# Kernel optimization log

Measured on AMD Instinct MI355X. Metric: run time of the kernel, lower is better.

## Reference

```python
import jax, jax.numpy as jnp
import numpy as np

D = 128          # hidden_channels
NU = 50000       # num user nodes
NI = 50000       # num item nodes
E = 600000       # edges per edge type
SLOPE = 0.01     # F.leaky_relu default negative_slope


def setup_inputs() -> dict:
    key = jax.random.key(0)
    ks = jax.random.split(key, 24)
    ws = 1.0 / np.sqrt(D)  # xavier-ish scale

    def W2(i):  # stacked [n_layers=2, D, D] weight
        return jax.random.normal(ks[i], (2, D, D), jnp.float32) * ws

    def B2(i):  # stacked [2, D] bias
        return jax.random.normal(ks[i], (2, D), jnp.float32) * 0.01

    inp = {
        "x_user": jax.random.normal(ks[0], (NU, D), jnp.float32),
        "x_item": jax.random.normal(ks[1], (NI, D), jnp.float32),
        # row 0 = src indices, row 1 = dst indices
        "ei_ui": jax.random.randint(ks[2], (2, E), 0, NU),  # user -> item (dst in [0,NI))
        "ei_iu": jax.random.randint(ks[3], (2, E), 0, NI),  # item -> user (dst in [0,NU))
        # per-node-type q/k/v Linear params, stacked over the 2 layers
        "q_w_user": W2(4),  "q_b_user": B2(5),
        "k_w_user": W2(6),  "k_b_user": B2(7),
        "v_w_user": W2(8),  "v_b_user": B2(9),
        "q_w_item": W2(10), "q_b_item": B2(11),
        "k_w_item": W2(12), "k_b_item": B2(13),
        "v_w_item": W2(14), "v_b_item": B2(15),
        # per-edge-type bilinear W, stacked over the 2 layers
        "W_ui": W2(16),
        "W_iu": W2(17),
    }
    return inp


def _edge_agg(x_src, x_dst, qw, qb, kw, kb, vw, vb, W, src, dst, n_dst):
    # torch Linear: x @ w.T + b
    q = x_src @ qw.T + qb            # [Nsrc, D]
    k = x_dst @ kw.T + kb            # [Ndst, D]
    v = x_src @ vw.T + vb            # [Nsrc, D]
    qW = q @ W                       # project on nodes (cheaper than per-edge)
    # per-edge bilinear score q_src . W . k_dst / sqrt(D)
    score = jnp.sum(qW[src] * k[dst], axis=-1) * (1.0 / np.sqrt(D))  # [E]
    alpha = jax.nn.softmax(jax.nn.leaky_relu(score, SLOPE))          # softmax over edges
    msg = alpha[:, None] * v[src]                                    # [E, D]
    return jax.ops.segment_sum(msg, dst, num_segments=n_dst)


def _layer(x_u, x_i, ei_ui, ei_iu, p, l):
    # edge type (user, rates, item): q/v from src type (user), k from dst type (item)
    agg_i = _edge_agg(x_u, x_i,
                      p["q_w_user"][l], p["q_b_user"][l],
                      p["k_w_item"][l], p["k_b_item"][l],
                      p["v_w_user"][l], p["v_b_user"][l],
                      p["W_ui"][l], ei_ui[0], ei_ui[1], NI)
    # edge type (item, rev_rates, user)
    agg_u = _edge_agg(x_i, x_u,
                      p["q_w_item"][l], p["q_b_item"][l],
                      p["k_w_user"][l], p["k_b_user"][l],
                      p["v_w_item"][l], p["v_b_item"][l],
                      p["W_iu"][l], ei_iu[0], ei_iu[1], NU)
    # out_dict initialized with x_dst.clone(), then scatter_add
    return x_u + agg_u, x_i + agg_i


def reference(x_user, x_item, ei_ui, ei_iu,
              q_w_user, q_b_user, k_w_user, k_b_user, v_w_user, v_b_user,
              q_w_item, q_b_item, k_w_item, k_b_item, v_w_item, v_b_item,
              W_ui, W_iu):
    p = dict(q_w_user=q_w_user, q_b_user=q_b_user, k_w_user=k_w_user,
             k_b_user=k_b_user, v_w_user=v_w_user, v_b_user=v_b_user,
             q_w_item=q_w_item, q_b_item=q_b_item, k_w_item=k_w_item,
             k_b_item=k_b_item, v_w_item=v_w_item, v_b_item=v_b_item,
             W_ui=W_ui, W_iu=W_iu)
    x_u, x_i = _layer(x_user, x_item, ei_ui, ei_iu, p, 0)  # conv1
    x_u, x_i = _layer(x_u, x_i, ei_ui, ei_iu, p, 1)        # conv2
    return jnp.concatenate([x_u, x_i], axis=0)  # [NU+NI, D]
```

## Files before the change

### kernel.cpp

```cpp
#include <hip/hip_runtime.h>
#include <stdint.h>

#define D 128

typedef __attribute__((ext_vector_type(8))) short bf16x8;
typedef __attribute__((ext_vector_type(4))) float f32x4;
typedef __attribute__((ext_vector_type(2))) float f32x2;
typedef unsigned short u16;
typedef unsigned char u8;
typedef unsigned int u32;

static __device__ __forceinline__ float b2f(u16 u) {
  return __uint_as_float(((unsigned)u) << 16);
}
static __device__ __forceinline__ u16 f2b(float f) {
  unsigned u = __float_as_uint(f);
  return (u16)((u + 0x7fffu + ((u >> 16) & 1u)) >> 16);
}

#if defined(__has_builtin)
#if __has_builtin(__builtin_amdgcn_cvt_pk_f32_fp8) && __has_builtin(__builtin_amdgcn_cvt_pk_fp8_f32)
#define HW_FP8 1
#endif
#endif

static __device__ __forceinline__ u8 enc_fp8(float f) {
#ifdef HW_FP8
  int p = __builtin_amdgcn_cvt_pk_fp8_f32(f, 0.f, 0, false);
  return (u8)(p & 0xff);
#else
  float a = fabsf(f);
  unsigned s = (__float_as_uint(f) >> 31) << 7;
  if (a < 7.8125e-3f) {
    int m = (int)(a * 512.f + 0.5f);
    if (m > 7) m = 7;
    return (u8)(s | m);
  }
  int e; float mant = frexpf(a, &e);
  int E = e + 6;
  int m = (int)((2.f * mant - 1.f) * 8.f + 0.5f);
  if (m == 8) { m = 0; E++; }
  if (E > 15 || (E == 15 && m > 6)) { E = 15; m = 6; }
  if (E < 1) return (u8)s;
  return (u8)(s | (E << 3) | m);
#endif
}

static __device__ __forceinline__ float dec1_fp8(u8 b) {
  int e = (b >> 3) & 15, m = b & 7;
  float mag = e ? ldexpf((float)(8 + m), e - 10) : ldexpf((float)m, -9);
  return (b & 128) ? -mag : mag;
}

static __device__ __forceinline__ void dec8_fp8(u32 lo, u32 hi, float* o) {
#ifdef HW_FP8
  f32x2 a = __builtin_amdgcn_cvt_pk_f32_fp8((int)lo, false);
  f32x2 b = __builtin_amdgcn_cvt_pk_f32_fp8((int)lo, true);
  f32x2 c = __builtin_amdgcn_cvt_pk_f32_fp8((int)hi, false);
  f32x2 d = __builtin_amdgcn_cvt_pk_f32_fp8((int)hi, true);
  o[0] = a.x; o[1] = a.y; o[2] = b.x; o[3] = b.y;
  o[4] = c.x; o[5] = c.y; o[6] = d.x; o[7] = d.y;
#else
  u32 w[2] = {lo, hi};
  u8* p = (u8*)w;
#pragma unroll
  for (int i = 0; i < 8; ++i) o[i] = dec1_fp8(p[i]);
#endif
}

__global__ void prep_fused(const float* __restrict__ qwu, const float* __restrict__ qbu,
                           const float* __restrict__ qwi, const float* __restrict__ qbi,
                           const float* __restrict__ Wui, const float* __restrict__ Wiu,
                           u16* __restrict__ Mt, float* __restrict__ bq) {
  int c = blockIdx.y, d = blockIdx.x, j = threadIdx.x;
  int l = c & 1, type = c >> 1;
  const float* qw = (type ? qwi : qwu) + l * D * D;
  const float* qb = (type ? qbi : qbu) + l * D;
  const float* W  = (type ? Wiu : Wui) + l * D * D;
  float acc = 0.f;
  for (int cc = 0; cc < D; ++cc) acc += qw[cc * D + d] * W[cc * D + j];
  Mt[((size_t)c * D + j) * D + d] = f2b(acc);
  if (d == 0) {
    float ba = 0.f;
    for (int cc = 0; cc < D; ++cc) ba += qb[cc] * W[cc * D + j];
    bq[c * D + j] = ba;
  }
}

__global__ void cast_w(const float* __restrict__ kwu, const float* __restrict__ kwi,
                       const float* __restrict__ vwu, const float* __restrict__ vwi,
                       u16* __restrict__ Wb) {
  int y = blockIdx.y;
  const float* s = (y == 0) ? kwu : (y == 1) ? kwi : (y == 2) ? vwu : vwi;
  int i = blockIdx.x * 256 + threadIdx.x;
  Wb[(size_t)y * 2 * D * D + i] = f2b(s[i]);
}

__global__ void cast_x(const float* __restrict__ x, u16* __restrict__ xb, int n2) {
  int i = blockIdx.x * 256 + threadIdx.x;
  if (i < n2) {
    float2 v = ((const float2*)x)[i];
    ((unsigned*)xb)[i] = (unsigned)f2b(v.x) | ((unsigned)f2b(v.y) << 16);
  }
}

__global__ void zero_i(int* __restrict__ p, int n) {
  int i = blockIdx.x * 256 + threadIdx.x;
  if (i < n) p[i] = 0;
}

__global__ __launch_bounds__(256) void bhist(const int* __restrict__ dui,
                                             const int* __restrict__ diu,
                                             int* __restrict__ cnt_ui,
                                             int* __restrict__ cnt_iu, int E) {
  __shared__ int h[256];
  int t = threadIdx.x;
  h[t] = 0;
  __syncthreads();
  const int* dp = blockIdx.y ? diu : dui;
  int e0 = blockIdx.x * 1024;
#pragma unroll
  for (int i = 0; i < 4; ++i) {
    int e = e0 + i * 256 + t;
    if (e < E) atomicAdd(&h[dp[e] >> 8], 1);
  }
  __syncthreads();
  int* out = blockIdx.y ? cnt_iu : cnt_ui;
  if (h[t]) atomicAdd(&out[t], h[t]);
}

__global__ __launch_bounds__(256) void bscan(const int* __restrict__ cnt_ui,
                                             const int* __restrict__ cnt_iu,
                                             int* __restrict__ base_ui, int* __restrict__ base_iu,
                                             int* __restrict__ cur_ui, int* __restrict__ cur_iu,
                                             int* __restrict__ rp_ui, int* __restrict__ rp_iu,
                                             int nb_ui, int nb_iu, int n_ui, int n_iu, int E) {
  __shared__ int sh[256];
  int t = threadIdx.x;
  int v = (t < nb_ui) ? cnt_ui[t] : 0;
  sh[t] = v;
  __syncthreads();
  for (int off = 1; off < 256; off <<= 1) {
    int u = (t >= off) ? sh[t - off] : 0;
    __syncthreads();
    sh[t] += u;
    __syncthreads();
  }
  int ex = sh[t] - v;
  if (t < nb_ui) { base_ui[t] = ex; cur_ui[t] = ex; }
  if (t == 0) { base_ui[nb_ui] = E; rp_ui[n_ui] = E; }
  __syncthreads();
  v = (t < nb_iu) ? cnt_iu[t] : 0;
  sh[t] = v;
  __syncthreads();
  for (int off = 1; off < 256; off <<= 1) {
    int u = (t >= off) ? sh[t - off] : 0;
    __syncthreads();
    sh[t] += u;
    __syncthreads();
  }
  ex = sh[t] - v;
  if (t < nb_iu) { base_iu[t] = ex; cur_iu[t] = ex; }
  if (t == 0) { base_iu[nb_iu] = E; rp_iu[n_iu] = E; }
}

__global__ __launch_bounds__(256) void bscatter(
    const int* __restrict__ sui, const int* __restrict__ dui,
    const int* __restrict__ siu, const int* __restrict__ diu,
    int* __restrict__ cur_ui, int* __restrict__ cur_iu,
    u32* __restrict__ bb_ui, u32* __restrict__ bb_iu, int E) {
  __shared__ int h[256], rbase[256], c2[256];
  int t = threadIdx.x;
  const int* sp = blockIdx.y ? siu : sui;
  const int* dp = blockIdx.y ? diu : dui;
  int* gc = blockIdx.y ? cur_iu : cur_ui;
  u32* bb = blockIdx.y ? bb_iu : bb_ui;
  h[t] = 0;
  c2[t] = 0;
  __syncthreads();
  int e0 = blockIdx.x * 1024;
  u32 pr[4];
  int bk[4];
  bool act[4];
#pragma unroll
  for (int i = 0; i < 4; ++i) {
    int e = e0 + i * 256 + t;
    act[i] = e < E;
    if (act[i]) {
      int s = sp[e], d2 = dp[e];
      pr[i] = ((u32)d2 << 16) | (u32)s;
      bk[i] = d2 >> 8;
      atomicAdd(&h[bk[i]], 1);
    }
  }
  __syncthreads();
  if (h[t]) rbase[t] = atomicAdd(&gc[t], h[t]);
  __syncthreads();
#pragma unroll
  for (int i = 0; i < 4; ++i) {
    if (act[i]) {
      int r = atomicAdd(&c2[bk[i]], 1);
      bb[rbase[bk[i]] + r] = pr[i];
    }
  }
}

__global__ __launch_bounds__(256) void bsort(
    const u32* __restrict__ bb_ui, const u32* __restrict__ bb_iu,
    const int* __restrict__ base_ui, const int* __restrict__ base_iu,
    int* __restrict__ rp_ui, int* __restrict__ rp_iu,
    int* __restrict__ cs_ui, int* __restrict__ cs_iu,
    int nb_ui, int n_ui, int n_iu) {
  int b = blockIdx.x;
  const u32* bb; const int* base; int* rp; int* cs; int n;
  if (b < nb_ui) { bb = bb_ui; base = base_ui; rp = rp_ui; cs = cs_ui; n = n_ui; }
  else { b -= nb_ui; bb = bb_iu; base = base_iu; rp = rp_iu; cs = cs_iu; n = n_iu; }
  int lo = base[b], hi = base[b + 1];
  __shared__ int h[256], sh[256], cur[256];
  int t = threadIdx.x;
  h[t] = 0;
  __syncthreads();
  for (int j = lo + t; j < hi; j += 256) atomicAdd(&h[(bb[j] >> 16) & 255], 1);
  __syncthreads();
  int v = h[t];
  sh[t] = v;
  __syncthreads();
  for (int off = 1; off < 256; off <<= 1) {
    int u = (t >= off) ? sh[t - off] : 0;
    __syncthreads();
    sh[t] += u;
    __syncthreads();
  }
  int ex = lo + sh[t] - v;
  int gd = (b << 8) + t;
  if (gd < n) rp[gd] = ex;
  cur[t] = ex;
  __syncthreads();
  for (int j = lo + t; j < hi; j += 256) {
    u32 pr = bb[j];
    int p = atomicAdd(&cur[(pr >> 16) & 255], 1);
    cs[p] = (int)(pr & 0xffffu);
  }
}

__global__ __launch_bounds__(256) void gemm3(
    const u16* __restrict__ xu, const u16* __restrict__ xi,
    const u16* __restrict__ wqu, const u16* __restrict__ wku, const u16* __restrict__ wvu,
    const float* __restrict__ bqu, const float* __restrict__ bku, const float* __restrict__ bvu,
    const u16* __restrict__ wqi, const u16* __restrict__ wki, const u16* __restrict__ wvi,
    const float* __restrict__ bqi, const float* __restrict__ bki, const float* __restrict__ bvi,
    u8* __restrict__ Tqv_u, u16* __restrict__ Tk_u,
    u8* __restrict__ Tqv_i, u16* __restrict__ Tk_i,
    int gu, int nu, int ni) {
  __shared__ __align__(16) u16 wlds[128 * 136];
  int bx = blockIdx.x, y = blockIdx.y;
  bool item = bx >= gu;
  if (item) bx -= gu;
  const u16* x = item ? xi : xu;
  int nrows = item ? ni : nu;
  const u16* wt; const float* bias;
  if (y == 0)      { wt = item ? wqi : wqu; bias = item ? bqi : bqu; }
  else if (y == 1) { wt = item ? wki : wku; bias = item ? bki : bku; }
  else             { wt = item ? wvi : wvu; bias = item ? bvi : bvu; }
  u8* Tqv = item ? Tqv_i : Tqv_u;
  u16* Tk = item ? Tk_i : Tk_u;

  int t = threadIdx.x;
#pragma unroll
  for (int i = 0; i < 8; ++i) {
    int idx = t + 256 * i;
    int n = idx >> 4, kc = idx & 15;
    ((bf16x8*)wlds)[n * 17 + kc] = ((const bf16x8*)wt)[idx];
  }
  __syncthreads();
  int wave = t >> 6, lane = t & 63;
  int m = lane & 15, quad = lane >> 4;
  int row0 = bx * 64 + wave * 16;
  int arow = row0 + m;
  const bf16x8* xv = (const bf16x8*)(x + (size_t)(arow < nrows ? arow : 0) * D);
  f32x4 acc[8];
#pragma unroll
  for (int n = 0; n < 8; ++n) acc[n] = (f32x4){0.f, 0.f, 0.f, 0.f};
#pragma unroll
  for (int kk = 0; kk < 4; ++kk) {
    bf16x8 a = xv[kk * 4 + quad];
#pragma unroll
    for (int n = 0; n < 8; ++n) {
      bf16x8 b = ((const bf16x8*)wlds)[(n * 16 + m) * 17 + kk * 4 + quad];
      acc[n] = __builtin_amdgcn_mfma_f32_16x16x32_bf16(a, b, acc[n], 0, 0, 0);
    }
  }
  if (y == 1) {
#pragma unroll
    for (int n = 0; n < 8; ++n) {
      float bb = bias[n * 16 + m];
#pragma unroll
      for (int r = 0; r < 4; ++r) {
        int orow = row0 + quad * 4 + r;
        if (orow < nrows) Tk[(size_t)orow * D + n * 16 + m] = f2b(acc[n][r] + bb);
      }
    }
  } else {
    int vo = (y == 0) ? 0 : 8;
#pragma unroll
    for (int n = 0; n < 8; ++n) {
      float bb = bias[n * 16 + m];
      int dim = n * 16 + m;
      int boff = ((dim >> 3) << 4) + (dim & 7) + vo;
#pragma unroll
      for (int r = 0; r < 4; ++r) {
        int orow = row0 + quad * 4 + r;
        if (orow < nrows) Tqv[(size_t)orow * 256 + boff] = enc_fp8(acc[n][r] + bb);
      }
    }
  }
}

__global__ __launch_bounds__(256) void agg_pass(
    const u8* __restrict__ Tqv_u, const u16* __restrict__ Tk_u,
    const u8* __restrict__ Tqv_i, const u16* __restrict__ Tk_i,
    const int* __restrict__ rp_ui, const int* __restrict__ cs_ui,
    const int* __restrict__ rp_iu, const int* __restrict__ cs_iu,
    float* __restrict__ agg_u, float* __restrict__ agg_i,
    float* __restrict__ zpart, int gai, int ni, int nu) {
  int bx = blockIdx.x;
  const u8* Pqv; const u16* Pk; const int* rp; const int* cs;
  float* agg; float* zp; int ndst;
  if (bx < gai) { Pqv = Tqv_u; Pk = Tk_i; rp = rp_ui; cs = cs_ui; agg = agg_i; zp = zpart; ndst = ni; }
  else { bx -= gai; Pqv = Tqv_i; Pk = Tk_u; rp = rp_iu; cs = cs_iu; agg = agg_u; zp = zpart + 1024; ndst = nu; }
  int wave = threadIdx.x >> 6, lane = threadIdx.x & 63;
  int d = bx * 4 + wave;
  int sub = lane & 15;
  int quad = lane >> 4;
  float z = 0.f;
  float acc[8] = {0.f, 0.f, 0.f, 0.f, 0.f, 0.f, 0.f, 0.f};
  if (d < ndst) {
    bf16x8 kf = *(const bf16x8*)(Pk + (size_t)d * D + sub * 8);
    float kx[8];
#pragma unroll
    for (int i = 0; i < 8; ++i) kx[i] = b2f((u16)((short*)&kf)[i]);
    int beg = rp[d], end = rp[d + 1];
    int iters = (end - beg + 3) >> 2;
    for (int it = 0; it < iters; ++it) {
      int j = beg + it * 4 + quad;
      bool act = j < end;
      int s = act ? cs[j] : 0;
      uint4 w = *(const uint4*)(Pqv + (size_t)s * 256 + sub * 16);
      float qx[8], vx[8];
      dec8_fp8(w.x, w.y, qx);
      dec8_fp8(w.z, w.w, vx);
      float dot = 0.f;
#pragma unroll
      for (int i = 0; i < 8; ++i) dot = fmaf(qx[i], kx[i], dot);
#pragma unroll
      for (int off = 1; off <= 8; off <<= 1) dot += __shfl_xor(dot, off, 64);
      float sc = dot * 0.08838834764831845f;
      sc = (sc > 0.f) ? sc : 0.01f * sc;
      float p = act ? __expf(sc) : 0.f;
      if (sub == 0) z += p;
#pragma unroll
      for (int i = 0; i < 8; ++i) acc[i] = fmaf(p, vx[i], acc[i]);
    }
#pragma unroll
    for (int i = 0; i < 8; ++i) {
      acc[i] += __shfl_xor(acc[i], 16, 64);
      acc[i] += __shfl_xor(acc[i], 32, 64);
    }
    if (quad == 0) {
      float* ap = agg + (size_t)d * D + sub * 8;
      ((f32x4*)ap)[0] = (f32x4){acc[0], acc[1], acc[2], acc[3]};
      ((f32x4*)ap)[1] = (f32x4){acc[4], acc[5], acc[6], acc[7]};
    }
    z += __shfl_xor(z, 16, 64);
    z += __shfl_xor(z, 32, 64);
  }
  __shared__ float ps[4];
  if (lane == 0) ps[wave] = z;
  __syncthreads();
  if (threadIdx.x == 0)
    unsafeAtomicAdd(&zp[blockIdx.x & 1023], ps[0] + ps[1] + ps[2] + ps[3]);
}

__global__ void zreduce(const float* __restrict__ zpart, float* __restrict__ zinv) {
  const float* zp = zpart + blockIdx.x * 1024;
  int t = threadIdx.x;
  float s = 0.f;
  for (int i = t; i < 1024; i += 256) s += zp[i];
  __shared__ float red[256];
  red[t] = s;
  __syncthreads();
  for (int k = 128; k > 0; k >>= 1) {
    if (t < k) red[t] += red[t + k];
    __syncthreads();
  }
  if (t == 0) zinv[blockIdx.x] = 1.0f / red[0];
}

__global__ void update_x(const float* __restrict__ xu, const float* __restrict__ xi,
                         const float* __restrict__ aggu, const float* __restrict__ aggi,
                         const float* __restrict__ zinv,
                         float* __restrict__ ou, float* __restrict__ oi,
                         u16* __restrict__ bu, u16* __restrict__ bi,
                         int nu, int ni, int wb) {
  int i = blockIdx.x * 256 + threadIdx.x;
  float zu = zinv[1];
  float zi = zinv[0];
  if (i < nu) {
    float v = xu[i] + aggu[i] * zu;
    ou[i] = v;
    if (wb) bu[i] = f2b(v);
  } else if (i < nu + ni) {
    int j = i - nu;
    float v = xi[j] + aggi[j] * zi;
    oi[j] = v;
    if (wb) bi[j] = f2b(v);
  }
}

extern "C" void kernel_launch(void* const* d_in, const int* in_sizes, int n_in,
                              void* d_out, int out_size, void* d_ws, size_t ws_size,
                              hipStream_t stream) {
  const float* xu_in = (const float*)d_in[0];
  const float* xi_in = (const float*)d_in[1];
  const int* ei_ui = (const int*)d_in[2];
  const int* ei_iu = (const int*)d_in[3];
  const float* qwu = (const float*)d_in[4];
  const float* qbu = (const float*)d_in[5];
  const float* kwu = (const float*)d_in[6];
  const float* kbu = (const float*)d_in[7];
  const float* vwu = (const float*)d_in[8];
  const float* vbu = (const float*)d_in[9];
  const float* qwi = (const float*)d_in[10];
  const float* qbi = (const float*)d_in[11];
  const float* kwi = (const float*)d_in[12];
  const float* kbi = (const float*)d_in[13];
  const float* vwi = (const float*)d_in[14];
  const float* vbi = (const float*)d_in[15];
  const float* Wui = (const float*)d_in[16];
  const float* Wiu = (const float*)d_in[17];

  int NU = in_sizes[0] / D;
  int NI = in_sizes[1] / D;
  int E  = in_sizes[2] / 2;

  char* w = (char*)d_ws;
  float* agg_u = (float*)w;  w += (size_t)NU * D * 4;
  float* agg_i = (float*)w;  w += (size_t)NI * D * 4;
  int* bcnt_ui = (int*)w;    w += 256 * 4;
  int* bcnt_iu = (int*)w;    w += 256 * 4;
  float* zpart = (float*)w;  w += 4096 * 4;
  float* zinv  = (float*)w;  w += 64;
  float* bq    = (float*)w;  w += 4 * D * 4;
  int* base_ui = (int*)w;    w += 260 * 4;
  int* base_iu = (int*)w;    w += 260 * 4;
  int* cur_ui  = (int*)w;    w += 256 * 4;
  int* cur_iu  = (int*)w;    w += 256 * 4;
  int* rp_ui = (int*)w;      w += (size_t)(NI + 4) * 4;
  int* rp_iu = (int*)w;      w += (size_t)(NU + 4) * 4;
  int* cs_ui = (int*)w;      w += (size_t)E * 4;
  int* cs_iu = (int*)w;      w += (size_t)E * 4;
  u32* bb_ui = (u32*)w;      w += (size_t)E * 4;
  u32* bb_iu = (u32*)w;      w += (size_t)E * 4;
  u16* Mt  = (u16*)w;        w += (size_t)4 * D * D * 2;
  u16* Wb  = (u16*)w;        w += (size_t)8 * D * D * 2;
  u16* xub = (u16*)w;        w += (size_t)NU * D * 2;
  u16* xib = (u16*)w;        w += (size_t)NI * D * 2;
  u16* Tk_u = (u16*)w;       w += (size_t)NU * D * 2;
  u16* Tk_i = (u16*)w;       w += (size_t)NI * D * 2;
  u8* Tqv_u = (u8*)w;        w += (size_t)NU * 256;
  u8* Tqv_i = (u8*)w;

  float* out_u = (float*)d_out;
  float* out_i = out_u + (size_t)NU * D;

  prep_fused<<<dim3(128, 4), 128, 0, stream>>>(qwu, qbu, qwi, qbi, Wui, Wiu, Mt, bq);
  cast_w<<<dim3(128, 4), 256, 0, stream>>>(kwu, kwi, vwu, vwi, Wb);
  cast_x<<<(NU * D / 2 + 255) / 256, 256, 0, stream>>>(xu_in, xub, NU * D / 2);
  cast_x<<<(NI * D / 2 + 255) / 256, 256, 0, stream>>>(xi_in, xib, NI * D / 2);

  int nb_ui = (NI + 255) >> 8;
  int nb_iu = (NU + 255) >> 8;
  zero_i<<<18, 256, 0, stream>>>(bcnt_ui, 512 + 4096);
  int geb = (E + 1023) / 1024;
  bhist<<<dim3(geb, 2), 256, 0, stream>>>(ei_ui + E, ei_iu + E, bcnt_ui, bcnt_iu, E);
  bscan<<<1, 256, 0, stream>>>(bcnt_ui, bcnt_iu, base_ui, base_iu, cur_ui, cur_iu,
                               rp_ui, rp_iu, nb_ui, nb_iu, NI, NU, E);
  bscatter<<<dim3(geb, 2), 256, 0, stream>>>(ei_ui, ei_ui + E, ei_iu, ei_iu + E,
                                             cur_ui, cur_iu, bb_ui, bb_iu, E);
  bsort<<<nb_ui + nb_iu, 256, 0, stream>>>(bb_ui, bb_iu, base_ui, base_iu,
                                           rp_ui, rp_iu, cs_ui, cs_iu, nb_ui, NI, NU);

  int gu = (NU + 63) / 64, gi = (NI + 63) / 64;
  int gau = (NU + 3) / 4, gai = (NI + 3) / 4;
  int gup = (NU * D + NI * D + 255) / 256;

  for (int l = 0; l < 2; ++l) {
    gemm3<<<dim3(gu + gi, 3), 256, 0, stream>>>(
        xub, xib,
        Mt + (size_t)l * D * D, Wb + (size_t)(0 + l) * D * D, Wb + (size_t)(4 + l) * D * D,
        bq + l * D, kbu + l * D, vbu + l * D,
        Mt + (size_t)(2 + l) * D * D, Wb + (size_t)(2 + l) * D * D, Wb + (size_t)(6 + l) * D * D,
        bq + (2 + l) * D, kbi + l * D, vbi + l * D,
        Tqv_u, Tk_u, Tqv_i, Tk_i, gu, NU, NI);
    agg_pass<<<gai + gau, 256, 0, stream>>>(
        Tqv_u, Tk_u, Tqv_i, Tk_i, rp_ui, cs_ui, rp_iu, cs_iu,
        agg_u, agg_i, zpart + (size_t)l * 2 * 1024, gai, NI, NU);
    zreduce<<<2, 256, 0, stream>>>(zpart + (size_t)l * 2 * 1024, zinv + l * 2);
    if (l == 0)
      update_x<<<gup, 256, 0, stream>>>(xu_in, xi_in, agg_u, agg_i, zinv + l * 2,
                                        out_u, out_i, xub, xib, NU * D, NI * D, 1);
    else
      update_x<<<gup, 256, 0, stream>>>(out_u, out_i, agg_u, agg_i, zinv + l * 2,
                                        out_u, out_i, nullptr, nullptr, NU * D, NI * D, 0);
  }
}
```

Measured before the change: 505.8 us.

## Batch neighbor index loads, issue three gathers per iteration, use DPP reductions

The aggregation loop now loads up to 64 neighbor indices with one coalesced read per wave and distributes them with shuffles. It then issues three independent row gathers per iteration before decoding them, which raises memory-level parallelism. The 16-lane dot-product reduction switches from ds_bpermute shuffles to DPP row operations. The costs are more registers per thread and some wasted masked work when the degree is not a multiple of 12.

```diff
diff --git a/kernel.cpp b/kernel.cpp
--- a/kernel.cpp
+++ b/kernel.cpp
@@ -66,6 +66,12 @@
 #pragma unroll
   for (int i = 0; i < 8; ++i) o[i] = dec1_fp8(p[i]);
 #endif
+}
+
+template <int CTRL>
+static __device__ __forceinline__ float dpp_add_f(float x) {
+  int y = __builtin_amdgcn_update_dpp(0, __float_as_int(x), CTRL, 0xf, 0xf, true);
+  return x + __int_as_float(y);
 }
 
 __global__ void prep_fused(const float* __restrict__ qwu, const float* __restrict__ qbu,
@@ -316,6 +322,26 @@
   }
 }
 
+static __device__ __forceinline__ void do_edge(uint4 w, bool act, const float* kx,
+                                               float* acc, float& z, int sub) {
+  float qx[8], vx[8];
+  dec8_fp8(w.x, w.y, qx);
+  dec8_fp8(w.z, w.w, vx);
+  float dot = 0.f;
+#pragma unroll
+  for (int i = 0; i < 8; ++i) dot = fmaf(qx[i], kx[i], dot);
+  dot = dpp_add_f<0xB1>(dot);
+  dot = dpp_add_f<0x4E>(dot);
+  dot = dpp_add_f<0x128>(dot);
+  dot = dpp_add_f<0x124>(dot);
+  float sc = dot * 0.08838834764831845f;
+  sc = (sc > 0.f) ? sc : 0.01f * sc;
+  float p = act ? __expf(sc) : 0.f;
+  if (sub == 0) z += p;
+#pragma unroll
+  for (int i = 0; i < 8; ++i) acc[i] = fmaf(p, vx[i], acc[i]);
+}
+
 __global__ __launch_bounds__(256) void agg_pass(
     const u8* __restrict__ Tqv_u, const u16* __restrict__ Tk_u,
     const u8* __restrict__ Tqv_i, const u16* __restrict__ Tk_i,
@@ -336,30 +362,28 @@
   float acc[8] = {0.f, 0.f, 0.f, 0.f, 0.f, 0.f, 0.f, 0.f};
   if (d < ndst) {
     bf16x8 kf = *(const bf16x8*)(Pk + (size_t)d * D + sub * 8);
+    int beg = rp[d], end = rp[d + 1];
+    int deg = end - beg;
     float kx[8];
 #pragma unroll
     for (int i = 0; i < 8; ++i) kx[i] = b2f((u16)((short*)&kf)[i]);
-    int beg = rp[d], end = rp[d + 1];
-    int iters = (end - beg + 3) >> 2;
-    for (int it = 0; it < iters; ++it) {
-      int j = beg + it * 4 + quad;
-      bool act = j < end;
-      int s = act ? cs[j] : 0;
-      uint4 w = *(const uint4*)(Pqv + (size_t)s * 256 + sub * 16);
-      float qx[8], vx[8];
-      dec8_fp8(w.x, w.y, qx);
-      dec8_fp8(w.z, w.w, vx);
-      float dot = 0.f;
-#pragma unroll
-      for (int i = 0; i < 8; ++i) dot = fmaf(qx[i], kx[i], dot);
-#pragma unroll
-      for (int off = 1; off <= 8; off <<= 1) dot += __shfl_xor(dot, off, 64);
-      float sc = dot * 0.08838834764831845f;
-      sc = (sc > 0.f) ? sc : 0.01f * sc;
-      float p = act ? __expf(sc) : 0.f;
-      if (sub == 0) z += p;
-#pragma unroll
-      for (int i = 0; i < 8; ++i) acc[i] = fmaf(p, vx[i], acc[i]);
+    const u8* Pq = Pqv + sub * 16;
+    for (int c0 = 0; c0 < deg; c0 += 64) {
+      int cdeg = deg - c0;
+      if (cdeg > 64) cdeg = 64;
+      int csv = (lane < cdeg) ? cs[beg + c0 + lane] : 0;
+      for (int b0 = 0; b0 < cdeg; b0 += 12) {
+        int i0 = b0 + quad, i1 = b0 + 4 + quad, i2 = b0 + 8 + quad;
+        int s0 = __shfl(csv, i0, 64);
+        int s1 = __shfl(csv, i1 < 64 ? i1 : 63, 64);
+        int s2 = __shfl(csv, i2 < 64 ? i2 : 63, 64);
+        uint4 w0 = *(const uint4*)(Pq + (size_t)s0 * 256);
+        uint4 w1 = *(const uint4*)(Pq + (size_t)s1 * 256);
+        uint4 w2 = *(const uint4*)(Pq + (size_t)s2 * 256);
+        do_edge(w0, i0 < cdeg, kx, acc, z, sub);
+        do_edge(w1, i1 < cdeg, kx, acc, z, sub);
+        do_edge(w2, i2 < cdeg, kx, acc, z, sub);
+      }
     }
 #pragma unroll
     for (int i = 0; i < 8; ++i) {
```

New measurement: 512.3 us. About the same (+1.3%).
